# Kernel optimization log

Hardware: AMD Instinct MI355X
Metric: run time of the kernel (lower is better)

The kernel has to match this reference:

```python
import math
import jax, jax.numpy as jnp
import numpy as np

D_MODEL = 256
N_HEADS = 8


def pos_embed_sine(h, w, num_pos_feats):
    """PositionEmbeddingSine with normalize=True; returns [2*num_pos_feats, h, w]."""
    scale = 2.0 * math.pi
    eps = 1e-6
    # cumsum of ones -> 1..h / 1..w
    y = (jnp.arange(1, h + 1, dtype=jnp.float32) - 0.5) / (h + eps) * scale
    x = (jnp.arange(1, w + 1, dtype=jnp.float32) - 0.5) / (w + eps) * scale
    i = jnp.arange(num_pos_feats, dtype=jnp.float32)
    dim_t = 10000.0 ** (2.0 * jnp.floor(i / 2.0) / num_pos_feats)
    px = x[:, None] / dim_t  # [w, F]
    py = y[:, None] / dim_t  # [h, F]

    def interleave(p):
        # stack(sin(even), cos(odd)) then flatten -> matches torch stack(...,dim=-1).flatten
        return jnp.stack([jnp.sin(p[:, 0::2]), jnp.cos(p[:, 1::2])], axis=-1).reshape(p.shape[0], -1)

    px = interleave(px)  # [w, F]
    py = interleave(py)  # [h, F]
    pos_y = jnp.broadcast_to(py[:, None, :], (h, w, num_pos_feats))
    pos_x = jnp.broadcast_to(px[None, :, :], (h, w, num_pos_feats))
    return jnp.concatenate([pos_y, pos_x], axis=-1).transpose(2, 0, 1)  # [2F, h, w]


def batched_attn_weights(q, k, Wq, bq, Wk, bk, nheads):
    """q,k: [N, S, E]. Returns head-averaged attention weights [N, L, S]
    (exactly what nn.MultiheadAttention returns with need_weights=True, eval mode)."""
    N, L, E = q.shape
    d = E // nheads
    inv = 1.0 / math.sqrt(d)
    qp = ((q @ Wq.T + bq) * inv).reshape(N, L, nheads, d).transpose(0, 2, 1, 3)   # [N,H,L,d]
    kp = (k @ Wk.T + bk).reshape(N, k.shape[1], nheads, d).transpose(0, 2, 1, 3)  # [N,H,S,d]
    scores = jnp.einsum('nhld,nhsd->nhls', qp, kp)
    w = jax.nn.softmax(scores, axis=-1)
    return w.mean(axis=1)  # average over heads -> [N,L,S]


def setup_inputs() -> dict:
    key = jax.random.key(0)
    k1, k2, k3, k4, k5 = jax.random.split(key, 5)
    x = jax.random.normal(k1, (5, D_MODEL, 80, 80), dtype=jnp.float32)
    in_proj_w = jax.random.normal(k2, (3 * D_MODEL, D_MODEL), dtype=jnp.float32) * 0.05
    in_proj_b = jax.random.normal(k3, (3 * D_MODEL,), dtype=jnp.float32) * 0.05
    sal_w = jax.random.normal(k4, (1,), dtype=jnp.float32)
    sal_b = jax.random.normal(k5, (1,), dtype=jnp.float32)
    return {"x": x, "in_proj_w": in_proj_w, "in_proj_b": in_proj_b,
            "sal_w": sal_w, "sal_b": sal_b}


def reference(x, in_proj_w, in_proj_b, sal_w, sal_b):
    b, c, h, w = x.shape  # b=5 (4 local + 1 global), c=d_model
    loc, glb = x[:4], x[4:5]
    ph, pw = h // 4, w // 4
    # 'n c (nh ph) (nw pw) -> (n nh nw) c ph pw' with nh=nw=4 -> 64 patches
    loc_p = loc.reshape(4, c, 4, ph, 4, pw).transpose(0, 2, 4, 1, 3, 5).reshape(64, c, ph, pw)
    pos = pos_embed_sine(ph, pw, c // 2)  # [c, ph, pw], identical for all patches
    query = (loc_p + pos).reshape(64, c, ph * pw).transpose(0, 2, 1)  # [64, L, c]
    # global branch: upsample x2 bilinear (align_corners=False), patch into 8x8 grid
    up_glb = jax.image.resize(glb, (1, c, 2 * h, 2 * w), method='bilinear')
    patched_glb = (up_glb.reshape(1, c, 8, ph, 8, pw)
                   .transpose(2, 4, 0, 1, 3, 5).reshape(64, c, ph, pw))
    key_t = (patched_glb + pos).reshape(64, c, ph * pw).transpose(0, 2, 1)  # [64, S, c]
    # single batched attention instead of 64 separate kernel launches
    Wq, Wk = in_proj_w[:c], in_proj_w[c:2 * c]
    bq, bk = in_proj_b[:c], in_proj_b[c:2 * c]
    aw = batched_attn_weights(query, key_t, Wq, bq, Wk, bk, N_HEADS)  # [64, L, S]
    aw_mean = aw.mean(axis=1)  # mean over query positions -> [64, S]
    # sal_conv is a 1x1 conv on a single channel == scalar affine
    imp = jax.nn.sigmoid(sal_w[0] * aw_mean.reshape(64, 1, ph, pw) + sal_b[0])
    # last_pred is None -> hist_importance initialized (torch.empty; defined here as zeros)
    current_importance = 0.6 * imp  # + 0.4 * zeros
    weighted = loc_p * current_importance  # broadcast [64,1,ph,pw]
    # '(n nh nw) c ph pw -> n c (nh ph) (nw pw)'
    loc_m = (weighted.reshape(4, 4, 4, c, ph, pw)
             .transpose(0, 3, 1, 4, 2, 5).reshape(4, c, h, w))
    # patches2image: '(hg wg b) c h w -> b c (hg h) (wg w)', hg=wg=2
    merged = (loc_m.reshape(2, 2, 1, c, h, w)
              .transpose(2, 3, 0, 4, 1, 5).reshape(1, c, 2 * h, 2 * w))
    return merged + up_glb * 0.5
```

## Files before the change

### kernel.cpp

```cpp
#include <hip/hip_runtime.h>
#include <math.h>

typedef __attribute__((ext_vector_type(8))) short bf16x8;
typedef __attribute__((ext_vector_type(8))) unsigned short u16x8;
typedef __attribute__((ext_vector_type(4))) float f32x4;
typedef unsigned short u16;


__device__ __forceinline__ u16 f2bf(float f){
  unsigned u = __float_as_uint(f);
  u += 0x7fffu + ((u >> 16) & 1u);
  return (u16)(u >> 16);
}

__device__ __forceinline__ float4 up4(const float* __restrict__ g, int Y, int X0){
  int jy = Y >> 1;
  int ry0, ry1; float wy0, wy1;
  if (Y & 1){ ry0 = jy; ry1 = (jy < 79) ? jy + 1 : 79; wy0 = 0.75f; wy1 = 0.25f; }
  else      { ry0 = (jy > 0) ? jy - 1 : 0; ry1 = jy;   wy0 = 0.25f; wy1 = 0.75f; }
  int jx = X0 >> 1;
  int cm1 = (jx > 0) ? jx - 1 : 0;
  int cp2 = (jx < 78) ? jx + 2 : 79;
  const float* r0 = g + ry0 * 80;
  const float* r1 = g + ry1 * 80;
  float cvm = wy0 * r0[cm1]  + wy1 * r1[cm1];
  float cv0 = wy0 * r0[jx]   + wy1 * r1[jx];
  float cv1 = wy0 * r0[jx+1] + wy1 * r1[jx+1];
  float cv2 = wy0 * r0[cp2]  + wy1 * r1[cp2];
  return make_float4(0.25f*cvm + 0.75f*cv0,
                     0.75f*cv0 + 0.25f*cv1,
                     0.25f*cv0 + 0.75f*cv1,
                     0.75f*cv1 + 0.25f*cv2);
}

__global__ __launch_bounds__(256) void pos_kernel(float* __restrict__ pos){
  int idx = blockIdx.x * 256 + threadIdx.x;
  int e = idx / 400, s = idx - e * 400;
  int y = s / 20, x = s - y * 20;
  int j = e & 127;
  int m = j >> 1;
  int k = (e < 128) ? y : x;
  float v = ((float)k + 0.5f) * (6.2831853071795864769f / 20.000001f);
  float invT = exp2f(-(float)m * 0.20762050593049448f);
  float arg = v * invT;
  pos[idx] = (j & 1) ? cosf(arg) : sinf(arg);
}

__global__ __launch_bounds__(256) void feat_kernel(const float* __restrict__ xin,
                                                   const float* __restrict__ pos,
                                                   u16* __restrict__ qf,
                                                   u16* __restrict__ kf){
  int which = blockIdx.y;
  int flat = blockIdx.x * 256 + threadIdx.x;
  int s4 = flat % 100;
  int rest = flat / 100;
  int e = rest & 255;
  int n = rest >> 8;
  int s0 = s4 * 4;
  int y = s0 / 20, x0 = s0 - y * 20;
  float4 pv = *(const float4*)(pos + e * 400 + s0);
  float4 val;
  u16* dst;
  if (which == 0){
    int img = n >> 4, pi = (n >> 2) & 3, pj = n & 3;
    const float* src = xin + (((img * 256 + e) * 80) + (pi * 20 + y)) * 80 + (pj * 20 + x0);
    float4 l = *(const float4*)src;
    val.x = l.x + pv.x; val.y = l.y + pv.y; val.z = l.z + pv.z; val.w = l.w + pv.w;
    dst = qf;
  } else {
    int gi = n >> 3, gj = n & 7;
    const float* g = xin + (4 * 256 + e) * 6400;
    float4 u = up4(g, gi * 20 + y, gj * 20 + x0);
    val.x = u.x + pv.x; val.y = u.y + pv.y; val.z = u.z + pv.z; val.w = u.w + pv.w;
    dst = kf;
  }
  ushort4 o;
  o.x = f2bf(val.x); o.y = f2bf(val.y); o.z = f2bf(val.z); o.w = f2bf(val.w);
  *(ushort4*)(dst + ((n * 256 + e) * 400 + s0)) = o;
}

__global__ __launch_bounds__(256) void proj_kernel(const u16* __restrict__ qf,
                                                   const u16* __restrict__ kf,
                                                   const float* __restrict__ W,
                                                   const float* __restrict__ bvec,
                                                   u16* __restrict__ qp,
                                                   u16* __restrict__ kp){
  __shared__ u16 lds_a[64 * 32];
  __shared__ u16 lds_b[400 * 32];

  int mat = blockIdx.y;
  int bx = blockIdx.x;
  int n = bx >> 2, ot = bx & 3;
  const u16* F = mat ? kf : qf;
  u16* O = mat ? kp : qp;
  const float* Wrow = W + (mat * 256 + ot * 64) * 256;
  const float* bias = bvec + mat * 256 + ot * 64;
  float scale = mat ? 1.0f : 0.17677669529663687f;

  int tid = threadIdx.x;
  int lane = tid & 63, wave = tid >> 6;
  int lo = lane & 15, hi = lane >> 4;

  float bl[4];
  #pragma unroll
  for (int r = 0; r < 4; r++) bl[r] = bias[wave * 16 + hi * 4 + r];

  f32x4 acc[25];
  #pragma unroll
  for (int t = 0; t < 25; t++) acc[t] = (f32x4){0.f, 0.f, 0.f, 0.f};

  for (int e0 = 0; e0 < 256; e0 += 32){
    __syncthreads();
    for (int c = tid; c < 512; c += 256){
      int row = c >> 3, e4 = c & 7;
      float4 w4 = *(const float4*)(Wrow + row * 256 + e0 + e4 * 4);
      ushort4 pk;
      pk.x = f2bf(w4.x); pk.y = f2bf(w4.y); pk.z = f2bf(w4.z); pk.w = f2bf(w4.w);
      int idx = row * 32 + ((e4 * 4) ^ ((row & 3) << 3));
      *(ushort4*)(lds_a + idx) = pk;
    }
    for (int c = tid; c < 1600; c += 256){
      int er = c & 31, s8 = c >> 5;
      u16x8 v = *(const u16x8*)(F + ((n * 256 + e0 + er) * 400 + s8 * 8));
      #pragma unroll
      for (int j = 0; j < 8; j++){
        int s = s8 * 8 + j;
        lds_b[s * 32 + (er ^ ((s & 3) << 3))] = v[j];
      }
    }
    __syncthreads();
    bf16x8 afr = *(const bf16x8*)(lds_a + (wave * 16 + lo) * 32 + ((hi * 8) ^ ((lo & 3) << 3)));
    #pragma unroll
    for (int st = 0; st < 25; st++){
      bf16x8 bfr = *(const bf16x8*)(lds_b + (st * 16 + lo) * 32 + ((hi * 8) ^ ((lo & 3) << 3)));
      acc[st] = __builtin_amdgcn_mfma_f32_16x16x32_bf16(afr, bfr, acc[st], 0, 0, 0);
    }
  }
  int o_loc = wave * 16 + hi * 4;
  int hh = ot * 2 + (o_loc >> 5);
  int d0 = o_loc & 31;
  #pragma unroll
  for (int st = 0; st < 25; st++){
    int s = st * 16 + lo;
    ushort4 pk;
    pk.x = f2bf((acc[st][0] + bl[0]) * scale);
    pk.y = f2bf((acc[st][1] + bl[1]) * scale);
    pk.z = f2bf((acc[st][2] + bl[2]) * scale);
    pk.w = f2bf((acc[st][3] + bl[3]) * scale);
    *(ushort4*)(O + ((size_t)((n * 8 + hh) * 400 + s)) * 32 + d0) = pk;
  }
}

__global__ __launch_bounds__(256) void attn_kernel(const u16* __restrict__ qp,
                                                   const u16* __restrict__ kp,
                                                   float* __restrict__ colsum){
  __shared__ float cs[400];

  int bx = blockIdx.x;
  int n = bx >> 3, h = bx & 7;
  int tid = threadIdx.x;
  for (int i = tid; i < 400; i += 256) cs[i] = 0.f;
  __syncthreads();

  int lane = tid & 63, wave = tid >> 6;
  int lo = lane & 15, hi = lane >> 4;

  const u16* qb = qp + (size_t)(n * 8 + h) * 400 * 32;
  const u16* kb = kp + (size_t)(n * 8 + h) * 400 * 32;

  float csacc[25][4];
  #pragma unroll
  for (int st = 0; st < 25; st++){
    #pragma unroll
    for (int r = 0; r < 4; r++) csacc[st][r] = 0.f;
  }

  for (int lt = wave; lt < 25; lt += 4){
    bf16x8 qfr = *(const bf16x8*)(qb + (lt * 16 + lo) * 32 + hi * 8);
    f32x4 sc[25];
    #pragma unroll
    for (int st = 0; st < 25; st++){
      bf16x8 kfr = *(const bf16x8*)(kb + (st * 16 + lo) * 32 + hi * 8);
      sc[st] = __builtin_amdgcn_mfma_f32_16x16x32_bf16(kfr, qfr, (f32x4){0.f, 0.f, 0.f, 0.f}, 0, 0, 0);
    }
    float m = -1e30f;
    #pragma unroll
    for (int st = 0; st < 25; st++){
      m = fmaxf(m, fmaxf(fmaxf(sc[st][0], sc[st][1]), fmaxf(sc[st][2], sc[st][3])));
    }
    m = fmaxf(m, __shfl_xor(m, 16, 64));
    m = fmaxf(m, __shfl_xor(m, 32, 64));
    float z = 0.f;
    #pragma unroll
    for (int st = 0; st < 25; st++){
      #pragma unroll
      for (int r = 0; r < 4; r++){
        float pv = __expf(sc[st][r] - m);
        sc[st][r] = pv;
        z += pv;
      }
    }
    z += __shfl_xor(z, 16, 64);
    z += __shfl_xor(z, 32, 64);
    float invz = 1.0f / z;
    #pragma unroll
    for (int st = 0; st < 25; st++){
      #pragma unroll
      for (int r = 0; r < 4; r++){
        csacc[st][r] += sc[st][r] * invz;
      }
    }
  }

  #pragma unroll
  for (int st = 0; st < 25; st++){
    #pragma unroll
    for (int r = 0; r < 4; r++){
      float wv = csacc[st][r];
      wv += __shfl_xor(wv, 1, 64);
      wv += __shfl_xor(wv, 2, 64);
      wv += __shfl_xor(wv, 4, 64);
      wv += __shfl_xor(wv, 8, 64);
      if (lo == 0) atomicAdd(&cs[st * 16 + hi * 4 + r], wv);
    }
  }
  __syncthreads();
  for (int i = tid; i < 400; i += 256)
    colsum[(n * 8 + h) * 400 + i] = cs[i];
}

__global__ __launch_bounds__(256) void imp_kernel(const float* __restrict__ colsum,
                                                  const float* __restrict__ sal_w,
                                                  const float* __restrict__ sal_b,
                                                  float* __restrict__ imp){
  int idx = blockIdx.x * 256 + threadIdx.x;
  int n = idx / 400, s = idx - n * 400;
  float sum = 0.f;
  #pragma unroll
  for (int h = 0; h < 8; h++) sum += colsum[(n * 8 + h) * 400 + s];
  float aw = sum * (1.0f / 3200.0f);
  float zz = sal_w[0] * aw + sal_b[0];
  imp[idx] = 1.0f / (1.0f + __expf(-zz));
}

__global__ __launch_bounds__(256) void out_kernel(const float* __restrict__ xin,
                                                  const float* __restrict__ imp,
                                                  float* __restrict__ out){
  int flat = blockIdx.x * 256 + threadIdx.x;
  int x4 = flat % 40;
  int rest = flat / 40;
  int Y = rest % 160;
  int e = rest / 160;
  int X0 = x4 * 4;
  int a = (Y >= 80) ? 1 : 0;
  int bq = (X0 >= 80) ? 1 : 0;
  int yy = Y - a * 80, xx = X0 - bq * 80;
  int pi = yy / 20, y = yy - pi * 20;
  int pj = xx / 20, x0 = xx - pj * 20;
  int img = a * 2 + bq;
  int nn = img * 16 + pi * 4 + pj;
  int s0 = y * 20 + x0;
  float4 l4 = *(const float4*)(xin + ((img * 256 + e) * 80 + yy) * 80 + xx);
  float4 i4 = *(const float4*)(imp + nn * 400 + s0);
  const float* g = xin + (4 * 256 + e) * 6400;
  float4 u4 = up4(g, Y, X0);
  float4 o;
  o.x = l4.x * (0.6f * i4.x) + 0.5f * u4.x;
  o.y = l4.y * (0.6f * i4.y) + 0.5f * u4.y;
  o.z = l4.z * (0.6f * i4.z) + 0.5f * u4.z;
  o.w = l4.w * (0.6f * i4.w) + 0.5f * u4.w;
  *(float4*)(out + (e * 160 + Y) * 160 + X0) = o;
}

extern "C" void kernel_launch(void* const* d_in, const int* in_sizes, int n_in,
                              void* d_out, int out_size, void* d_ws, size_t ws_size,
                              hipStream_t stream) {
  const float* x      = (const float*)d_in[0];
  const float* W      = (const float*)d_in[1];
  const float* bvec   = (const float*)d_in[2];
  const float* sal_w  = (const float*)d_in[3];
  const float* sal_b  = (const float*)d_in[4];
  float* out = (float*)d_out;

  const size_t POS_OFF = 0;
  const size_t QF_OFF  = 409600;
  const size_t KF_OFF  = QF_OFF + 13107200;
  const size_t QP_OFF  = KF_OFF + 13107200;
  const size_t KP_OFF  = QP_OFF + 13107200;
  const size_t CS_OFF  = KP_OFF + 13107200;
  const size_t IMP_OFF = CS_OFF + 819200;
  const size_t NEED    = IMP_OFF + 102400;
  if (ws_size < NEED) return;

  char* ws = (char*)d_ws;
  float* pos    = (float*)(ws + POS_OFF);
  u16*   qf     = (u16*)(ws + QF_OFF);
  u16*   kf     = (u16*)(ws + KF_OFF);
  u16*   qp     = (u16*)(ws + QP_OFF);
  u16*   kp     = (u16*)(ws + KP_OFF);
  float* colsum = (float*)(ws + CS_OFF);
  float* imp    = (float*)(ws + IMP_OFF);

  pos_kernel<<<400, 256, 0, stream>>>(pos);
  feat_kernel<<<dim3(6400, 2), 256, 0, stream>>>(x, pos, qf, kf);
  proj_kernel<<<dim3(256, 2), 256, 0, stream>>>(qf, kf, W, bvec, qp, kp);
  attn_kernel<<<512, 256, 0, stream>>>(qp, kp, colsum);
  imp_kernel<<<100, 256, 0, stream>>>(colsum, sal_w, sal_b, imp);
  out_kernel<<<6400, 256, 0, stream>>>(x, imp, out);
}
```

Measured before the change: 135.9 us.

## Stage Q/K tiles in LDS and use exp2 softmax without max subtraction

The attention kernel now copies each head's Q and K tiles into shared memory once (K with a padded row stride), instead of re-reading K from global memory for every query tile. The softmax also folds log2(e) into the query scale and uses exp2 directly. It drops the running-max pass and its cross-lane shuffles, and splits the sum into four independent accumulators. Without the max subtraction, exp2 can overflow if scores grow large, and the larger shared-memory footprint may cut occupancy.

```diff
diff --git a/kernel.cpp b/kernel.cpp
--- a/kernel.cpp
+++ b/kernel.cpp
@@ -95,7 +95,7 @@
   u16* O = mat ? kp : qp;
   const float* Wrow = W + (mat * 256 + ot * 64) * 256;
   const float* bias = bvec + mat * 256 + ot * 64;
-  float scale = mat ? 1.0f : 0.17677669529663687f;
+  float scale = mat ? 1.0f : 0.25505419776f;
 
   int tid = threadIdx.x;
   int lane = tid & 63, wave = tid >> 6;
@@ -154,20 +154,34 @@
 __global__ __launch_bounds__(256) void attn_kernel(const u16* __restrict__ qp,
                                                    const u16* __restrict__ kp,
                                                    float* __restrict__ colsum){
+  __shared__ u16 q_lds[400 * 32];
+  __shared__ u16 k_lds[400 * 40];
   __shared__ float cs[400];
 
   int bx = blockIdx.x;
   int n = bx >> 3, h = bx & 7;
   int tid = threadIdx.x;
   for (int i = tid; i < 400; i += 256) cs[i] = 0.f;
+
+  const u16* qb = qp + (size_t)(n * 8 + h) * 400 * 32;
+  const u16* kb = kp + (size_t)(n * 8 + h) * 400 * 32;
+
+  for (int c = tid; c < 3200; c += 256){
+    int chunk = c & 3, row = c >> 2;
+    if (row < 400){
+      u16x8 v = *(const u16x8*)(qb + row * 32 + chunk * 8);
+      *(u16x8*)(q_lds + row * 32 + chunk * 8) = v;
+    } else {
+      int r2 = row - 400;
+      u16x8 v = *(const u16x8*)(kb + r2 * 32 + chunk * 8);
+      *(u16x8*)(k_lds + r2 * 40 + chunk * 8) = v;
+    }
+  }
   __syncthreads();
 
   int lane = tid & 63, wave = tid >> 6;
   int lo = lane & 15, hi = lane >> 4;
 
-  const u16* qb = qp + (size_t)(n * 8 + h) * 400 * 32;
-  const u16* kb = kp + (size_t)(n * 8 + h) * 400 * 32;
-
   float csacc[25][4];
   #pragma unroll
   for (int st = 0; st < 25; st++){
@@ -176,30 +190,24 @@
   }
 
   for (int lt = wave; lt < 25; lt += 4){
-    bf16x8 qfr = *(const bf16x8*)(qb + (lt * 16 + lo) * 32 + hi * 8);
+    bf16x8 qfr = *(const bf16x8*)(q_lds + (lt * 16 + lo) * 32 + hi * 8);
     f32x4 sc[25];
     #pragma unroll
     for (int st = 0; st < 25; st++){
-      bf16x8 kfr = *(const bf16x8*)(kb + (st * 16 + lo) * 32 + hi * 8);
+      bf16x8 kfr = *(const bf16x8*)(k_lds + (st * 16 + lo) * 40 + hi * 8);
       sc[st] = __builtin_amdgcn_mfma_f32_16x16x32_bf16(kfr, qfr, (f32x4){0.f, 0.f, 0.f, 0.f}, 0, 0, 0);
     }
-    float m = -1e30f;
+    float z0 = 0.f, z1 = 0.f, z2 = 0.f, z3 = 0.f;
     #pragma unroll
     for (int st = 0; st < 25; st++){
-      m = fmaxf(m, fmaxf(fmaxf(sc[st][0], sc[st][1]), fmaxf(sc[st][2], sc[st][3])));
-    }
-    m = fmaxf(m, __shfl_xor(m, 16, 64));
-    m = fmaxf(m, __shfl_xor(m, 32, 64));
-    float z = 0.f;
-    #pragma unroll
-    for (int st = 0; st < 25; st++){
-      #pragma unroll
-      for (int r = 0; r < 4; r++){
-        float pv = __expf(sc[st][r] - m);
-        sc[st][r] = pv;
-        z += pv;
-      }
-    }
+      float p0 = exp2f(sc[st][0]);
+      float p1 = exp2f(sc[st][1]);
+      float p2 = exp2f(sc[st][2]);
+      float p3 = exp2f(sc[st][3]);
+      sc[st][0] = p0; sc[st][1] = p1; sc[st][2] = p2; sc[st][3] = p3;
+      z0 += p0; z1 += p1; z2 += p2; z3 += p3;
+    }
+    float z = (z0 + z1) + (z2 + z3);
     z += __shfl_xor(z, 16, 64);
     z += __shfl_xor(z, 32, 64);
     float invz = 1.0f / z;
```

Result: slower. 147.7 us (+8.7%).

## Restructure attention column-sum into two-pass key-resident kernel split over query halves

Applied to the files above, without the earlier changes.

The attention kernel now keeps each wave's key fragments in registers. It runs two passes over query tiles: the first computes softmax row normalisers, and the second recomputes the scores and accumulates normalised column sums. The log2(e) factor is folded into the query scale so exp2f can be used, and the running-max subtraction is dropped. Query rows are split across two blocks per (n, head), and partial column sums are written without LDS atomics. The aim is lower register pressure and higher occupancy than the old 25-tile score arrays. In exchange the MFMA work is done twice, and skipping the max subtraction risks overflow if score magnitudes are large.

```diff
diff --git a/kernel.cpp b/kernel.cpp
--- a/kernel.cpp
+++ b/kernel.cpp
@@ -95,7 +95,7 @@
   u16* O = mat ? kp : qp;
   const float* Wrow = W + (mat * 256 + ot * 64) * 256;
   const float* bias = bvec + mat * 256 + ot * 64;
-  float scale = mat ? 1.0f : 0.17677669529663687f;
+  float scale = mat ? 1.0f : 0.25505419776f;
 
   int tid = threadIdx.x;
   int lane = tid & 63, wave = tid >> 6;
@@ -153,83 +153,91 @@
 
 __global__ __launch_bounds__(256) void attn_kernel(const u16* __restrict__ qp,
                                                    const u16* __restrict__ kp,
-                                                   float* __restrict__ colsum){
-  __shared__ float cs[400];
+                                                   float* __restrict__ colsum2){
+  __shared__ float zp[4 * 208];
+  __shared__ float invzl[208];
 
   int bx = blockIdx.x;
-  int n = bx >> 3, h = bx & 7;
+  int yhalf = blockIdx.y;
+  int lt0 = yhalf ? 13 : 0;
+  int nl  = yhalf ? 12 : 13;
   int tid = threadIdx.x;
-  for (int i = tid; i < 400; i += 256) cs[i] = 0.f;
-  __syncthreads();
-
-  int lane = tid & 63, wave = tid >> 6;
+  int lane = tid & 63, w = tid >> 6;
   int lo = lane & 15, hi = lane >> 4;
 
-  const u16* qb = qp + (size_t)(n * 8 + h) * 400 * 32;
-  const u16* kb = kp + (size_t)(n * 8 + h) * 400 * 32;
-
-  float csacc[25][4];
-  #pragma unroll
-  for (int st = 0; st < 25; st++){
-    #pragma unroll
-    for (int r = 0; r < 4; r++) csacc[st][r] = 0.f;
-  }
-
-  for (int lt = wave; lt < 25; lt += 4){
+  const u16* qb = qp + (size_t)bx * 400 * 32;
+  const u16* kb = kp + (size_t)bx * 400 * 32;
+
+  bf16x8 kfr[7];
+  #pragma unroll
+  for (int j = 0; j < 7; j++){
+    int st = w + 4 * j;
+    if (st < 25) kfr[j] = *(const bf16x8*)(kb + (st * 16 + lo) * 32 + hi * 8);
+  }
+
+  for (int li = 0; li < nl; li++){
+    int lt = lt0 + li;
     bf16x8 qfr = *(const bf16x8*)(qb + (lt * 16 + lo) * 32 + hi * 8);
-    f32x4 sc[25];
-    #pragma unroll
-    for (int st = 0; st < 25; st++){
-      bf16x8 kfr = *(const bf16x8*)(kb + (st * 16 + lo) * 32 + hi * 8);
-      sc[st] = __builtin_amdgcn_mfma_f32_16x16x32_bf16(kfr, qfr, (f32x4){0.f, 0.f, 0.f, 0.f}, 0, 0, 0);
-    }
-    float m = -1e30f;
-    #pragma unroll
-    for (int st = 0; st < 25; st++){
-      m = fmaxf(m, fmaxf(fmaxf(sc[st][0], sc[st][1]), fmaxf(sc[st][2], sc[st][3])));
-    }
-    m = fmaxf(m, __shfl_xor(m, 16, 64));
-    m = fmaxf(m, __shfl_xor(m, 32, 64));
     float z = 0.f;
     #pragma unroll
-    for (int st = 0; st < 25; st++){
+    for (int j = 0; j < 7; j++){
+      int st = w + 4 * j;
+      if (st < 25){
+        f32x4 sc = __builtin_amdgcn_mfma_f32_16x16x32_bf16(kfr[j], qfr, (f32x4){0.f,0.f,0.f,0.f}, 0, 0, 0);
+        z += (exp2f(sc[0]) + exp2f(sc[1])) + (exp2f(sc[2]) + exp2f(sc[3]));
+      }
+    }
+    z += __shfl_xor(z, 16, 64);
+    z += __shfl_xor(z, 32, 64);
+    if (hi == 0) zp[w * 208 + li * 16 + lo] = z;
+  }
+  __syncthreads();
+  for (int i = tid; i < nl * 16; i += 256)
+    invzl[i] = 1.0f / (((zp[i] + zp[208 + i]) + (zp[416 + i] + zp[624 + i])));
+  __syncthreads();
+
+  float csacc[7][4];
+  #pragma unroll
+  for (int j = 0; j < 7; j++){
+    #pragma unroll
+    for (int r = 0; r < 4; r++) csacc[j][r] = 0.f;
+  }
+  for (int li = 0; li < nl; li++){
+    int lt = lt0 + li;
+    bf16x8 qfr = *(const bf16x8*)(qb + (lt * 16 + lo) * 32 + hi * 8);
+    float wl = invzl[li * 16 + lo];
+    #pragma unroll
+    for (int j = 0; j < 7; j++){
+      int st = w + 4 * j;
+      if (st < 25){
+        f32x4 sc = __builtin_amdgcn_mfma_f32_16x16x32_bf16(kfr[j], qfr, (f32x4){0.f,0.f,0.f,0.f}, 0, 0, 0);
+        csacc[j][0] += exp2f(sc[0]) * wl;
+        csacc[j][1] += exp2f(sc[1]) * wl;
+        csacc[j][2] += exp2f(sc[2]) * wl;
+        csacc[j][3] += exp2f(sc[3]) * wl;
+      }
+    }
+  }
+
+  #pragma unroll
+  for (int j = 0; j < 7; j++){
+    int st = w + 4 * j;
+    if (st < 25){
       #pragma unroll
       for (int r = 0; r < 4; r++){
-        float pv = __expf(sc[st][r] - m);
-        sc[st][r] = pv;
-        z += pv;
+        float v = csacc[j][r];
+        v += __shfl_xor(v, 1, 64);
+        v += __shfl_xor(v, 2, 64);
+        v += __shfl_xor(v, 4, 64);
+        v += __shfl_xor(v, 8, 64);
+        if (lo == 0)
+          colsum2[((size_t)(yhalf * 512 + bx)) * 400 + st * 16 + hi * 4 + r] = v;
       }
     }
-    z += __shfl_xor(z, 16, 64);
-    z += __shfl_xor(z, 32, 64);
-    float invz = 1.0f / z;
-    #pragma unroll
-    for (int st = 0; st < 25; st++){
-      #pragma unroll
-      for (int r = 0; r < 4; r++){
-        csacc[st][r] += sc[st][r] * invz;
-      }
-    }
-  }
-
-  #pragma unroll
-  for (int st = 0; st < 25; st++){
-    #pragma unroll
-    for (int r = 0; r < 4; r++){
-      float wv = csacc[st][r];
-      wv += __shfl_xor(wv, 1, 64);
-      wv += __shfl_xor(wv, 2, 64);
-      wv += __shfl_xor(wv, 4, 64);
-      wv += __shfl_xor(wv, 8, 64);
-      if (lo == 0) atomicAdd(&cs[st * 16 + hi * 4 + r], wv);
-    }
-  }
-  __syncthreads();
-  for (int i = tid; i < 400; i += 256)
-    colsum[(n * 8 + h) * 400 + i] = cs[i];
-}
-
-__global__ __launch_bounds__(256) void imp_kernel(const float* __restrict__ colsum,
+  }
+}
+
+__global__ __launch_bounds__(256) void imp_kernel(const float* __restrict__ colsum2,
                                                   const float* __restrict__ sal_w,
                                                   const float* __restrict__ sal_b,
                                                   float* __restrict__ imp){
@@ -237,7 +245,10 @@
   int n = idx / 400, s = idx - n * 400;
   float sum = 0.f;
   #pragma unroll
-  for (int h = 0; h < 8; h++) sum += colsum[(n * 8 + h) * 400 + s];
+  for (int h = 0; h < 8; h++){
+    sum += colsum2[(size_t)(n * 8 + h) * 400 + s];
+    sum += colsum2[(size_t)(512 + n * 8 + h) * 400 + s];
+  }
   float aw = sum * (1.0f / 3200.0f);
   float zz = sal_w[0] * aw + sal_b[0];
   imp[idx] = 1.0f / (1.0f + __expf(-zz));
@@ -288,7 +299,7 @@
   const size_t QP_OFF  = KF_OFF + 13107200;
   const size_t KP_OFF  = QP_OFF + 13107200;
   const size_t CS_OFF  = KP_OFF + 13107200;
-  const size_t IMP_OFF = CS_OFF + 819200;
+  const size_t IMP_OFF = CS_OFF + 1638400;
   const size_t NEED    = IMP_OFF + 102400;
   if (ws_size < NEED) return;
 
@@ -298,13 +309,13 @@
   u16*   kf     = (u16*)(ws + KF_OFF);
   u16*   qp     = (u16*)(ws + QP_OFF);
   u16*   kp     = (u16*)(ws + KP_OFF);
-  float* colsum = (float*)(ws + CS_OFF);
+  float* colsum2= (float*)(ws + CS_OFF);
   float* imp    = (float*)(ws + IMP_OFF);
 
   pos_kernel<<<400, 256, 0, stream>>>(pos);
   feat_kernel<<<dim3(6400, 2), 256, 0, stream>>>(x, pos, qf, kf);
   proj_kernel<<<dim3(256, 2), 256, 0, stream>>>(qf, kf, W, bvec, qp, kp);
-  attn_kernel<<<512, 256, 0, stream>>>(qp, kp, colsum);
-  imp_kernel<<<100, 256, 0, stream>>>(colsum, sal_w, sal_b, imp);
+  attn_kernel<<<dim3(512, 2), 256, 0, stream>>>(qp, kp, colsum2);
+  imp_kernel<<<100, 256, 0, stream>>>(colsum2, sal_w, sal_b, imp);
   out_kernel<<<6400, 256, 0, stream>>>(x, imp, out);
 }
```

Measured after the change: 124.9 us. 1.09x faster.
